# Optimization experiments

Measured on AMD Instinct MI355X. Metric: run time of the kernel, lower is better.

## Reference

```python
import jax, jax.numpy as jnp
import numpy as np

N_NODES = 50000
N_EDGES = 800000
D_IN, D_HID, D_OUT = 64, 128, 64


def _sage_conv(x, src, dst, W_l, b_l, W_r):
    # PyG SAGEConv (aggr='mean'): out = lin_l(mean_j x_j) + lin_r(x_i)
    msg = x[src]                                    # [E, d] gather
    summed = jax.ops.segment_sum(msg, dst, num_segments=N_NODES)
    cnt = jax.ops.segment_sum(jnp.ones((msg.shape[0], 1), x.dtype), dst,
                              num_segments=N_NODES)
    mean = summed / jnp.maximum(cnt, 1.0)           # [N, d]
    return mean @ W_l + b_l + x @ W_r


def setup_inputs() -> dict:
    key = jax.random.key(0)
    ks = jax.random.split(key, 8)
    x = jax.random.normal(ks[0], (N_NODES, D_IN), dtype=jnp.float32)
    edge_index = jax.random.randint(ks[1], (2, N_EDGES), 0, N_NODES, dtype=jnp.int64)
    s1 = 1.0 / np.sqrt(D_IN)
    s2 = 1.0 / np.sqrt(D_HID)
    W_l1 = jax.random.uniform(ks[2], (D_IN, D_HID), jnp.float32, -s1, s1)
    b_l1 = jnp.zeros((D_HID,), jnp.float32)
    W_r1 = jax.random.uniform(ks[3], (D_IN, D_HID), jnp.float32, -s1, s1)
    W_l2 = jax.random.uniform(ks[4], (D_HID, D_OUT), jnp.float32, -s2, s2)
    b_l2 = jnp.zeros((D_OUT,), jnp.float32)
    W_r2 = jax.random.uniform(ks[5], (D_HID, D_OUT), jnp.float32, -s2, s2)
    return {"x": x, "edge_index": edge_index,
            "W_l1": W_l1, "b_l1": b_l1, "W_r1": W_r1,
            "W_l2": W_l2, "b_l2": b_l2, "W_r2": W_r2}


def reference(x, edge_index, W_l1, b_l1, W_r1, W_l2, b_l2, W_r2):
    src, dst = edge_index[0], edge_index[1]
    h = _sage_conv(x, src, dst, W_l1, b_l1, W_r1)
    h = jax.nn.relu(h)
    # dropout is identity in eval mode (F.dropout(training=self.training))
    out = _sage_conv(h, src, dst, W_l2, b_l2, W_r2)
    return out
```

## Files before the change

kernel.cpp:

```cpp
#include <hip/hip_runtime.h>

namespace {

constexpr int NNODES = 50000;
constexpr int NEDGES = 800000;
constexpr int NBUCK  = (NNODES + 127) / 128;
constexpr int BCAP   = 3072;
constexpr int SB     = 64;
constexpr int CHUNK  = NEDGES / SB;
constexpr int CONVB  = 1024;


static __device__ __forceinline__ unsigned short f2bf(float f) {
  unsigned u = __float_as_uint(f);
  u += 0x7FFFu + ((u >> 16) & 1u);
  return (unsigned short)(u >> 16);
}
static __device__ __forceinline__ float bf2f(unsigned short b) {
  return __uint_as_float((unsigned)b << 16);
}

static __device__ __forceinline__ void pk_fma_lo(float2& d, const float2 a, const float2 b) {
  asm("v_pk_fma_f32 %0, %1, %2, %0 op_sel:[0,0,0] op_sel_hi:[0,1,1]"
      : "+v"(d) : "v"(a), "v"(b));
}
static __device__ __forceinline__ void pk_fma_hi(float2& d, const float2 a, const float2 b) {
  asm("v_pk_fma_f32 %0, %1, %2, %0 op_sel:[1,0,0] op_sel_hi:[1,1,1]"
      : "+v"(d) : "v"(a), "v"(b));
}

static __device__ __forceinline__ int detect_is64_block(const void* raw, int* s_tmp) {
  if (threadIdx.x == 0) *s_tmp = 0;
  __syncthreads();
  const unsigned int* w = (const unsigned int*)raw;
  const int nz = (w[1 + 2 * (int)(threadIdx.x & 511)] != 0u) ? 1 : 0;
  if (nz) atomicOr(s_tmp, 1);
  __syncthreads();
  return (*s_tmp == 0) ? 1 : 0;
}

__global__ __launch_bounds__(512) void histconv(const void* __restrict__ raw,
                                                const float* __restrict__ xin,
                                                unsigned short* __restrict__ xb,
                                                int* __restrict__ blkhist) {
  const int tid = (int)threadIdx.x;
  if (blockIdx.x >= SB) {
    const int b = blockIdx.x - SB;
    for (int t = b * 512 + tid; t < NNODES * 64 / 4; t += CONVB * 512) {
      const float4 v = ((const float4*)xin)[t];
      ushort4 o;
      o.x = f2bf(v.x); o.y = f2bf(v.y); o.z = f2bf(v.z); o.w = f2bf(v.w);
      ((ushort4*)xb)[t] = o;
    }
    return;
  }
  __shared__ int hist[NBUCK];
  __shared__ int s_tmp;
  const int is64 = detect_is64_block(raw, &s_tmp);
  for (int i = tid; i < NBUCK; i += 512) hist[i] = 0;
  __syncthreads();
  const int b = blockIdx.x;
  const int beg = b * CHUNK, end = beg + CHUNK;
  for (int e = beg + tid; e < end; e += 512) {
    const int d = is64 ? (int)((const long long*)raw)[NEDGES + e]
                       : ((const int*)raw)[NEDGES + e];
    atomicAdd(&hist[d >> 7], 1);
  }
  __syncthreads();
  for (int i = tid; i < NBUCK; i += 512) blkhist[i * SB + b] = hist[i];
}

__global__ __launch_bounds__(512) void scatter_pass(const void* __restrict__ raw,
                                                    const int* __restrict__ blkhist,
                                                    unsigned int* __restrict__ ecol) {
  __shared__ int loff[NBUCK];
  __shared__ int lcur[NBUCK];
  __shared__ int s_tmp;
  const int is64 = detect_is64_block(raw, &s_tmp);
  const int b = blockIdx.x;
  const int tid = (int)threadIdx.x;
  for (int bk = tid; bk < NBUCK; bk += 512) {
    int s = 0;
    for (int bb = 0; bb < b; ++bb) s += blkhist[bk * SB + bb];
    loff[bk] = bk * BCAP + s;
    lcur[bk] = 0;
  }
  __syncthreads();
  const int beg = b * CHUNK, end = beg + CHUNK;
  for (int e = beg + tid; e < end; e += 512) {
    int s, d;
    if (is64) {
      const long long* p = (const long long*)raw;
      s = (int)p[e];
      d = (int)p[NEDGES + e];
    } else {
      const int* p = (const int*)raw;
      s = p[e];
      d = p[NEDGES + e];
    }
    const int bk = d >> 7;
    const unsigned int val = ((unsigned int)d << 16) | (unsigned int)s;
    const int lr = atomicAdd(&lcur[bk], 1);
    ecol[loff[bk] + lr] = val;
  }
}

__global__ __launch_bounds__(256) void csr_emit(const int* __restrict__ blkhist,
                                                unsigned int* __restrict__ ecol,
                                                int* __restrict__ rowse) {
  const int bk = blockIdx.x;
  const int base = bk * 128;
  const int nloc = min(128, NNODES - base);
  const int tid = (int)threadIdx.x;
  unsigned int* eb = ecol + (size_t)bk * BCAP;

  __shared__ int dcnt[128];
  __shared__ int noff[128];
  __shared__ int ncur[128];
  __shared__ int s_cnt;
  if (tid < 64) {
    int c = blkhist[bk * SB + tid];
#pragma unroll
    for (int off = 32; off; off >>= 1) c += __shfl_down(c, off, 64);
    if (tid == 0) s_cnt = c;
  }
  if (tid < 128) dcnt[tid] = 0;
  __syncthreads();
  const int cnt = s_cnt;

  unsigned int vals[12];
  int m = 0;
#pragma unroll
  for (int k = 0; k < 12; ++k) {
    const int e = tid + k * 256;
    if (e < cnt) {
      vals[k] = eb[e];
      atomicAdd(&dcnt[(vals[k] >> 16) & 127u], 1);
      m = k + 1;
    }
  }
  __syncthreads();

  if (tid < 128) noff[tid] = dcnt[tid];
  __syncthreads();
#pragma unroll
  for (int off = 1; off < 128; off <<= 1) {
    int add = 0;
    if (tid < 128 && tid >= off) add = noff[tid - off];
    __syncthreads();
    if (tid < 128) noff[tid] += add;
    __syncthreads();
  }
  if (tid < 128) {
    const int excl = noff[tid] - dcnt[tid];
    noff[tid] = excl;
    ncur[tid] = 0;
    if (tid < nloc)
      rowse[base + tid] = ((bk * BCAP + excl) << 9) | dcnt[tid];
  }
  __syncthreads();

#pragma unroll
  for (int k = 0; k < 12; ++k) {
    if (k < m) {
      const int loc = (int)((vals[k] >> 16) & 127u);
      eb[noff[loc] + atomicAdd(&ncur[loc], 1)] = vals[k] & 0xFFFFu;
    }
  }
}

template <bool FINAL>
__global__ __launch_bounds__(256) void seg_mean_bf(const unsigned int* __restrict__ xb2,
                                                   const int* __restrict__ rowse,
                                                   const unsigned int* __restrict__ col,
                                                   const unsigned int* __restrict__ radd2,
                                                   float* __restrict__ outbuf) {
  const int lane = (int)(threadIdx.x & 63);
  const int half = lane >> 5;
  const int c = lane & 31;
  const int wid = (blockIdx.x * blockDim.x + threadIdx.x) >> 6;
  const int nw = (gridDim.x * blockDim.x) >> 6;
  for (int v = wid; v < NNODES; v += nw) {
    const int se = rowse[v];
    const int b = se >> 9;
    const int e = b + (se & 511);
    float accx = 0.0f, accy = 0.0f;
    int i = b;
    for (; i + 8 <= e; i += 8) {
      const int s0 = (int)col[i + 0 + half];
      const int s1 = (int)col[i + 2 + half];
      const int s2 = (int)col[i + 4 + half];
      const int s3 = (int)col[i + 6 + half];
      const unsigned int w0 = xb2[(size_t)s0 * 32 + c];
      const unsigned int w1 = xb2[(size_t)s1 * 32 + c];
      const unsigned int w2 = xb2[(size_t)s2 * 32 + c];
      const unsigned int w3 = xb2[(size_t)s3 * 32 + c];
      accx += __uint_as_float(w0 << 16) + __uint_as_float(w1 << 16)
            + __uint_as_float(w2 << 16) + __uint_as_float(w3 << 16);
      accy += __uint_as_float(w0 & 0xFFFF0000u) + __uint_as_float(w1 & 0xFFFF0000u)
            + __uint_as_float(w2 & 0xFFFF0000u) + __uint_as_float(w3 & 0xFFFF0000u);
    }
    for (; i + 2 <= e; i += 2) {
      const unsigned int w0 = xb2[(size_t)col[i + half] * 32 + c];
      accx += __uint_as_float(w0 << 16);
      accy += __uint_as_float(w0 & 0xFFFF0000u);
    }
    if (i < e && half == 0) {
      const unsigned int w0 = xb2[(size_t)col[i] * 32 + c];
      accx += __uint_as_float(w0 << 16);
      accy += __uint_as_float(w0 & 0xFFFF0000u);
    }
    accx += __shfl_xor(accx, 32, 64);
    accy += __shfl_xor(accy, 32, 64);
    if (half == 0) {
      const float inv = 1.0f / fmaxf((float)(se & 511), 1.0f);
      float2 res = make_float2(accx * inv, accy * inv);
      const size_t gi = (size_t)v * 32 + c;
      if (FINAL) {
        const unsigned int ra = radd2[gi];
        res.x += __uint_as_float(ra << 16);
        res.y += __uint_as_float(ra & 0xFFFF0000u);
      }
      ((float2*)outbuf)[gi] = res;
    }
  }
}

template <int MODE>
__global__ __launch_bounds__(256, 4) void gemm128(const float* __restrict__ A0,
                                                  const float* __restrict__ A1,
                                                  const unsigned short* __restrict__ AH,
                                                  const float* __restrict__ W0,
                                                  const float* __restrict__ W1,
                                                  const float* __restrict__ bias,
                                                  unsigned short* __restrict__ HB,
                                                  unsigned short* __restrict__ PB,
                                                  unsigned short* __restrict__ RB) {
  constexpr int SAS = 36;
  __shared__ float sA[64][SAS];
  __shared__ float sW[32][128];
  const int row0 = blockIdx.x * 64;
  const int tid = threadIdx.x;
  const int r0 = (tid >> 4) * 4;
  const int j0 = (tid & 15) * 4;

  float2 accA2[4][2];
  float2 accB2[4][2];
#pragma unroll
  for (int r = 0; r < 4; ++r)
#pragma unroll
    for (int p = 0; p < 2; ++p) {
      accA2[r][p] = make_float2(0.f, 0.f);
      accB2[r][p] = make_float2(0.f, 0.f);
    }

#pragma unroll 1
  for (int ck = 0; ck < 4; ++ck) {
#pragma unroll
    for (int v = 0; v < 2; ++v) {
      const int vid = v * 256 + tid;
      const int rr = vid >> 3;
      const int kq = (vid & 7) * 4;
      const int grow = row0 + rr;
      float4 val = make_float4(0.f, 0.f, 0.f, 0.f);
      if (grow < NNODES) {
        if (MODE == 0) {
          const float* src = (ck < 2) ? A0 : A1;
          const int kk = (ck & 1) * 32 + kq;
          val = *(const float4*)&src[(size_t)grow * 64 + kk];
        } else {
          const ushort4 us = *(const ushort4*)&AH[(size_t)grow * 128 + ck * 32 + kq];
          val = make_float4(bf2f(us.x), bf2f(us.y), bf2f(us.z), bf2f(us.w));
        }
      }
      *(float4*)&sA[rr][kq] = val;
    }
#pragma unroll
    for (int v = 0; v < 4; ++v) {
      const int vid = v * 256 + tid;
      const int kk = vid >> 5;
      const int jq = (vid & 31) * 4;
      float4 w;
      if (MODE == 0) {
        const float* src = (ck < 2) ? W0 : W1;
        const int krel = (ck & 1) * 32 + kk;
        w = *(const float4*)&src[(size_t)krel * 128 + jq];
      } else {
        const int kg = ck * 32 + kk;
        const float* src = (jq < 64) ? W0 : W1;
        const int jrel = (jq < 64) ? jq : jq - 64;
        w = *(const float4*)&src[(size_t)kg * 64 + jrel];
      }
      *(float4*)&sW[kk][jq] = w;
    }
    __syncthreads();
#pragma unroll
    for (int k4 = 0; k4 < 8; ++k4) {
      float4 a[4];
#pragma unroll
      for (int r = 0; r < 4; ++r) a[r] = *(const float4*)&sA[r0 + r][k4 * 4];
#pragma unroll
      for (int kp = 0; kp < 2; ++kp) {
        const int k_even = k4 * 4 + kp * 2;
        const float4 wlo0 = *(const float4*)&sW[k_even][j0];
        const float4 whi0 = *(const float4*)&sW[k_even][64 + j0];
        const float4 wlo1 = *(const float4*)&sW[k_even + 1][j0];
        const float4 whi1 = *(const float4*)&sW[k_even + 1][64 + j0];
#pragma unroll
        for (int r = 0; r < 4; ++r) {
          const float2 ap = (kp == 0) ? make_float2(a[r].x, a[r].y)
                                      : make_float2(a[r].z, a[r].w);
          pk_fma_lo(accA2[r][0], ap, make_float2(wlo0.x, wlo0.y));
          pk_fma_lo(accA2[r][1], ap, make_float2(wlo0.z, wlo0.w));
          pk_fma_lo(accB2[r][0], ap, make_float2(whi0.x, whi0.y));
          pk_fma_lo(accB2[r][1], ap, make_float2(whi0.z, whi0.w));
          pk_fma_hi(accA2[r][0], ap, make_float2(wlo1.x, wlo1.y));
          pk_fma_hi(accA2[r][1], ap, make_float2(wlo1.z, wlo1.w));
          pk_fma_hi(accB2[r][0], ap, make_float2(whi1.x, whi1.y));
          pk_fma_hi(accB2[r][1], ap, make_float2(whi1.z, whi1.w));
        }
      }
    }
    __syncthreads();
  }

  float4 blo = make_float4(0.f, 0.f, 0.f, 0.f);
  float4 bhi;
  if (MODE == 0) {
    blo = *(const float4*)&bias[j0];
    bhi = *(const float4*)&bias[64 + j0];
  } else {
    bhi = *(const float4*)&bias[j0];
  }
#pragma unroll
  for (int r = 0; r < 4; ++r) {
    const int grow = row0 + r0 + r;
    if (grow >= NNODES) continue;
    float4 lo = make_float4(accA2[r][0].x + blo.x, accA2[r][0].y + blo.y,
                            accA2[r][1].x + blo.z, accA2[r][1].y + blo.w);
    float4 hi = make_float4(accB2[r][0].x + bhi.x, accB2[r][0].y + bhi.y,
                            accB2[r][1].x + bhi.z, accB2[r][1].y + bhi.w);
    if (MODE == 0) {
      ushort4 olo, ohi;
      olo.x = f2bf(fmaxf(lo.x, 0.f)); olo.y = f2bf(fmaxf(lo.y, 0.f));
      olo.z = f2bf(fmaxf(lo.z, 0.f)); olo.w = f2bf(fmaxf(lo.w, 0.f));
      ohi.x = f2bf(fmaxf(hi.x, 0.f)); ohi.y = f2bf(fmaxf(hi.y, 0.f));
      ohi.z = f2bf(fmaxf(hi.z, 0.f)); ohi.w = f2bf(fmaxf(hi.w, 0.f));
      *(ushort4*)&HB[(size_t)grow * 128 + j0] = olo;
      *(ushort4*)&HB[(size_t)grow * 128 + 64 + j0] = ohi;
    } else {
      ushort4 op, orr;
      op.x = f2bf(lo.x); op.y = f2bf(lo.y); op.z = f2bf(lo.z); op.w = f2bf(lo.w);
      orr.x = f2bf(hi.x); orr.y = f2bf(hi.y); orr.z = f2bf(hi.z); orr.w = f2bf(hi.w);
      *(ushort4*)&PB[(size_t)grow * 64 + j0] = op;
      *(ushort4*)&RB[(size_t)grow * 64 + j0] = orr;
    }
  }
}

}

extern "C" void kernel_launch(void* const* d_in, const int* in_sizes, int n_in,
                              void* d_out, int out_size, void* d_ws, size_t ws_size,
                              hipStream_t stream) {
  const float* x   = (const float*)d_in[0];
  const void*  ei  = d_in[1];
  const float* Wl1 = (const float*)d_in[2];
  const float* bl1 = (const float*)d_in[3];
  const float* Wr1 = (const float*)d_in[4];
  const float* Wl2 = (const float*)d_in[5];
  const float* bl2 = (const float*)d_in[6];
  const float* Wr2 = (const float*)d_in[7];
  float* out = (float*)d_out;

  char* ws = (char*)d_ws;
  int*            blkhist = (int*)(ws + 0);
  int*            rowse   = (int*)(ws + 100352);
  unsigned int*   ecol    = (unsigned int*)(ws + 301056);
  unsigned short* xb      = (unsigned short*)(ws + 5105664);
  unsigned short* pb      = (unsigned short*)(ws + 11505664);
  float*          mean1   = (float*)(ws + 17905664);
  unsigned short* hb      = (unsigned short*)(ws + 30705664);
  unsigned short* rb      = (unsigned short*)(ws + 43505664);

  histconv<<<SB + CONVB, 512, 0, stream>>>(ei, x, xb, blkhist);
  scatter_pass<<<SB, 512, 0, stream>>>(ei, blkhist, ecol);
  csr_emit<<<NBUCK, 256, 0, stream>>>(blkhist, ecol, rowse);

  constexpr int GEMM_BLOCKS = (NNODES + 63) / 64;

  seg_mean_bf<false><<<12500, 256, 0, stream>>>((const unsigned int*)xb, rowse, ecol,
                                                nullptr, mean1);
  gemm128<0><<<GEMM_BLOCKS, 256, 0, stream>>>(mean1, x, nullptr, Wl1, Wr1, bl1,
                                              hb, nullptr, nullptr);
  gemm128<1><<<GEMM_BLOCKS, 256, 0, stream>>>(nullptr, nullptr, hb, Wl2, Wr2, bl2,
                                              nullptr, pb, rb);
  seg_mean_bf<true><<<12500, 256, 0, stream>>>((const unsigned int*)pb, rowse, ecol,
                                               (const unsigned int*)rb, out);
}
```

Baseline: 158.2 us.

## Replace FP32 FMA GEMMs with bf16 MFMA using split hi/lo weights

Both dense GEMMs now run on MFMA 16x16x32 bf16 instructions instead of scalar packed FP32 FMAs. Weights are pre-transposed and split into bf16 hi and lo parts inside the first kernel, so precision stays near FP32 for the weights. The first-layer mean aggregate is now written as bf16 rather than fp32, and layer 1 reads the bf16 copy of x, which halves those activation reads and writes. The cost is extra rounding on the activations and two MFMAs per k-step, and the weight B fragments are read straight from global memory.

```diff
diff --git a/kernel.cpp b/kernel.cpp
--- a/kernel.cpp
+++ b/kernel.cpp
@@ -11,6 +11,9 @@
 constexpr int CONVB  = 1024;
 
 
+typedef __attribute__((ext_vector_type(8))) short bf16x8;
+typedef __attribute__((ext_vector_type(4))) float f32x4;
+
 static __device__ __forceinline__ unsigned short f2bf(float f) {
   unsigned u = __float_as_uint(f);
   u += 0x7FFFu + ((u >> 16) & 1u);
@@ -20,15 +23,6 @@
   return __uint_as_float((unsigned)b << 16);
 }
 
-static __device__ __forceinline__ void pk_fma_lo(float2& d, const float2 a, const float2 b) {
-  asm("v_pk_fma_f32 %0, %1, %2, %0 op_sel:[0,0,0] op_sel_hi:[0,1,1]"
-      : "+v"(d) : "v"(a), "v"(b));
-}
-static __device__ __forceinline__ void pk_fma_hi(float2& d, const float2 a, const float2 b) {
-  asm("v_pk_fma_f32 %0, %1, %2, %0 op_sel:[1,0,0] op_sel_hi:[1,1,1]"
-      : "+v"(d) : "v"(a), "v"(b));
-}
-
 static __device__ __forceinline__ int detect_is64_block(const void* raw, int* s_tmp) {
   if (threadIdx.x == 0) *s_tmp = 0;
   __syncthreads();
@@ -41,9 +35,38 @@
 
 __global__ __launch_bounds__(512) void histconv(const void* __restrict__ raw,
                                                 const float* __restrict__ xin,
+                                                const float* __restrict__ Wl1,
+                                                const float* __restrict__ Wr1,
+                                                const float* __restrict__ Wl2,
+                                                const float* __restrict__ Wr2,
                                                 unsigned short* __restrict__ xb,
+                                                unsigned short* __restrict__ WT1hi,
+                                                unsigned short* __restrict__ WT1lo,
+                                                unsigned short* __restrict__ WT2hi,
+                                                unsigned short* __restrict__ WT2lo,
                                                 int* __restrict__ blkhist) {
   const int tid = (int)threadIdx.x;
+  if (blockIdx.x >= SB + CONVB) {
+    const int q = (int)blockIdx.x - (SB + CONVB);
+    const int layer = q >> 1;
+    const int jbase = (q & 1) * 64;
+    unsigned short* WH = layer ? WT2hi : WT1hi;
+    unsigned short* WL = layer ? WT2lo : WT1lo;
+    for (int t = tid; t < 64 * 128; t += 512) {
+      const int j = jbase + (t >> 7);
+      const int k = t & 127;
+      float wv;
+      if (layer == 0) wv = (k < 64) ? Wl1[(size_t)k * 128 + j]
+                                    : Wr1[(size_t)(k - 64) * 128 + j];
+      else            wv = (j < 64) ? Wl2[(size_t)k * 64 + j]
+                                    : Wr2[(size_t)k * 64 + (j - 64)];
+      const unsigned short hi = f2bf(wv);
+      const unsigned short lo = f2bf(wv - bf2f(hi));
+      WH[(size_t)j * 128 + k] = hi;
+      WL[(size_t)j * 128 + k] = lo;
+    }
+    return;
+  }
   if (blockIdx.x >= SB) {
     const int b = blockIdx.x - SB;
     for (int t = b * 512 + tid; t < NNODES * 64 / 4; t += CONVB * 512) {
@@ -174,7 +197,8 @@
                                                    const int* __restrict__ rowse,
                                                    const unsigned int* __restrict__ col,
                                                    const unsigned int* __restrict__ radd2,
-                                                   float* __restrict__ outbuf) {
+                                                   float* __restrict__ outf,
+                                                   unsigned int* __restrict__ outb) {
   const int lane = (int)(threadIdx.x & 63);
   const int half = lane >> 5;
   const int c = lane & 31;
@@ -220,140 +244,102 @@
         const unsigned int ra = radd2[gi];
         res.x += __uint_as_float(ra << 16);
         res.y += __uint_as_float(ra & 0xFFFF0000u);
+        ((float2*)outf)[gi] = res;
+      } else {
+        outb[gi] = ((unsigned)f2bf(res.y) << 16) | (unsigned)f2bf(res.x);
       }
-      ((float2*)outbuf)[gi] = res;
     }
   }
 }
 
 template <int MODE>
-__global__ __launch_bounds__(256, 4) void gemm128(const float* __restrict__ A0,
-                                                  const float* __restrict__ A1,
-                                                  const unsigned short* __restrict__ AH,
-                                                  const float* __restrict__ W0,
-                                                  const float* __restrict__ W1,
-                                                  const float* __restrict__ bias,
-                                                  unsigned short* __restrict__ HB,
-                                                  unsigned short* __restrict__ PB,
-                                                  unsigned short* __restrict__ RB) {
-  constexpr int SAS = 36;
-  __shared__ float sA[64][SAS];
-  __shared__ float sW[32][128];
+__global__ __launch_bounds__(256, 4) void gemm_mfma(const unsigned short* __restrict__ A0,
+                                                    const unsigned short* __restrict__ A1,
+                                                    const unsigned short* __restrict__ WThi,
+                                                    const unsigned short* __restrict__ WTlo,
+                                                    const float* __restrict__ bias,
+                                                    unsigned short* __restrict__ O0,
+                                                    unsigned short* __restrict__ O1) {
+  constexpr int LDA = 136;
+  constexpr int LDO = 132;
+  __shared__ unsigned short At[64 * LDA];
   const int row0 = blockIdx.x * 64;
-  const int tid = threadIdx.x;
-  const int r0 = (tid >> 4) * 4;
-  const int j0 = (tid & 15) * 4;
-
-  float2 accA2[4][2];
-  float2 accB2[4][2];
-#pragma unroll
-  for (int r = 0; r < 4; ++r)
-#pragma unroll
-    for (int p = 0; p < 2; ++p) {
-      accA2[r][p] = make_float2(0.f, 0.f);
-      accB2[r][p] = make_float2(0.f, 0.f);
-    }
+  const int tid = (int)threadIdx.x;
+
+#pragma unroll
+  for (int cc = 0; cc < 4; ++cc) {
+    const int chunk = cc * 256 + tid;
+    const int rr = chunk >> 4;
+    const int seg = chunk & 15;
+    const int grow = row0 + rr;
+    ushort4 v0 = make_ushort4(0, 0, 0, 0), v1 = make_ushort4(0, 0, 0, 0);
+    if (grow < NNODES) {
+      const unsigned short* src;
+      if (MODE == 0)
+        src = (seg < 8) ? &A0[(size_t)grow * 64 + seg * 8]
+                        : &A1[(size_t)grow * 64 + (seg - 8) * 8];
+      else
+        src = &A0[(size_t)grow * 128 + seg * 8];
+      v0 = *(const ushort4*)src;
+      v1 = *(const ushort4*)(src + 4);
+    }
+    *(ushort4*)&At[rr * LDA + seg * 8] = v0;
+    *(ushort4*)&At[rr * LDA + seg * 8 + 4] = v1;
+  }
+  __syncthreads();
+
+  const int w = tid >> 6;
+  const int l = tid & 63;
+  const int i16 = l & 15;
+  const int g = l >> 4;
+
+  bf16x8 af[4];
+#pragma unroll
+  for (int ks = 0; ks < 4; ++ks)
+    af[ks] = *(const bf16x8*)&At[(w * 16 + i16) * LDA + ks * 32 + g * 8];
+  __syncthreads();
 
 #pragma unroll 1
-  for (int ck = 0; ck < 4; ++ck) {
-#pragma unroll
-    for (int v = 0; v < 2; ++v) {
-      const int vid = v * 256 + tid;
-      const int rr = vid >> 3;
-      const int kq = (vid & 7) * 4;
-      const int grow = row0 + rr;
-      float4 val = make_float4(0.f, 0.f, 0.f, 0.f);
-      if (grow < NNODES) {
-        if (MODE == 0) {
-          const float* src = (ck < 2) ? A0 : A1;
-          const int kk = (ck & 1) * 32 + kq;
-          val = *(const float4*)&src[(size_t)grow * 64 + kk];
-        } else {
-          const ushort4 us = *(const ushort4*)&AH[(size_t)grow * 128 + ck * 32 + kq];
-          val = make_float4(bf2f(us.x), bf2f(us.y), bf2f(us.z), bf2f(us.w));
-        }
-      }
-      *(float4*)&sA[rr][kq] = val;
-    }
-#pragma unroll
-    for (int v = 0; v < 4; ++v) {
-      const int vid = v * 256 + tid;
-      const int kk = vid >> 5;
-      const int jq = (vid & 31) * 4;
-      float4 w;
-      if (MODE == 0) {
-        const float* src = (ck < 2) ? W0 : W1;
-        const int krel = (ck & 1) * 32 + kk;
-        w = *(const float4*)&src[(size_t)krel * 128 + jq];
-      } else {
-        const int kg = ck * 32 + kk;
-        const float* src = (jq < 64) ? W0 : W1;
-        const int jrel = (jq < 64) ? jq : jq - 64;
-        w = *(const float4*)&src[(size_t)kg * 64 + jrel];
-      }
-      *(float4*)&sW[kk][jq] = w;
-    }
-    __syncthreads();
-#pragma unroll
-    for (int k4 = 0; k4 < 8; ++k4) {
-      float4 a[4];
-#pragma unroll
-      for (int r = 0; r < 4; ++r) a[r] = *(const float4*)&sA[r0 + r][k4 * 4];
-#pragma unroll
-      for (int kp = 0; kp < 2; ++kp) {
-        const int k_even = k4 * 4 + kp * 2;
-        const float4 wlo0 = *(const float4*)&sW[k_even][j0];
-        const float4 whi0 = *(const float4*)&sW[k_even][64 + j0];
-        const float4 wlo1 = *(const float4*)&sW[k_even + 1][j0];
-        const float4 whi1 = *(const float4*)&sW[k_even + 1][64 + j0];
-#pragma unroll
-        for (int r = 0; r < 4; ++r) {
-          const float2 ap = (kp == 0) ? make_float2(a[r].x, a[r].y)
-                                      : make_float2(a[r].z, a[r].w);
-          pk_fma_lo(accA2[r][0], ap, make_float2(wlo0.x, wlo0.y));
-          pk_fma_lo(accA2[r][1], ap, make_float2(wlo0.z, wlo0.w));
-          pk_fma_lo(accB2[r][0], ap, make_float2(whi0.x, whi0.y));
-          pk_fma_lo(accB2[r][1], ap, make_float2(whi0.z, whi0.w));
-          pk_fma_hi(accA2[r][0], ap, make_float2(wlo1.x, wlo1.y));
-          pk_fma_hi(accA2[r][1], ap, make_float2(wlo1.z, wlo1.w));
-          pk_fma_hi(accB2[r][0], ap, make_float2(whi1.x, whi1.y));
-          pk_fma_hi(accB2[r][1], ap, make_float2(whi1.z, whi1.w));
-        }
-      }
-    }
-    __syncthreads();
-  }
-
-  float4 blo = make_float4(0.f, 0.f, 0.f, 0.f);
-  float4 bhi;
-  if (MODE == 0) {
-    blo = *(const float4*)&bias[j0];
-    bhi = *(const float4*)&bias[64 + j0];
-  } else {
-    bhi = *(const float4*)&bias[j0];
-  }
-#pragma unroll
-  for (int r = 0; r < 4; ++r) {
-    const int grow = row0 + r0 + r;
+  for (int ct = 0; ct < 8; ++ct) {
+    f32x4 acc = {0.f, 0.f, 0.f, 0.f};
+    const size_t wb = (size_t)(ct * 16 + i16) * 128 + g * 8;
+#pragma unroll
+    for (int ks = 0; ks < 4; ++ks) {
+      const bf16x8 bh = *(const bf16x8*)&WThi[wb + ks * 32];
+      acc = __builtin_amdgcn_mfma_f32_16x16x32_bf16(af[ks], bh, acc, 0, 0, 0);
+      const bf16x8 bl = *(const bf16x8*)&WTlo[wb + ks * 32];
+      acc = __builtin_amdgcn_mfma_f32_16x16x32_bf16(af[ks], bl, acc, 0, 0, 0);
+    }
+    const int colc = ct * 16 + i16;
+    float bsc = 0.f;
+    if (MODE == 0) bsc = bias[colc];
+    else if (colc >= 64) bsc = bias[colc - 64];
+#pragma unroll
+    for (int e = 0; e < 4; ++e) {
+      float v = acc[e] + bsc;
+      if (MODE == 0) v = fmaxf(v, 0.f);
+      At[(w * 16 + g * 4 + e) * LDO + colc] = f2bf(v);
+    }
+  }
+  __syncthreads();
+
+#pragma unroll
+  for (int cc = 0; cc < 4; ++cc) {
+    const int chunk = cc * 256 + tid;
+    const int rr = chunk >> 4;
+    const int seg = chunk & 15;
+    const int grow = row0 + rr;
     if (grow >= NNODES) continue;
-    float4 lo = make_float4(accA2[r][0].x + blo.x, accA2[r][0].y + blo.y,
-                            accA2[r][1].x + blo.z, accA2[r][1].y + blo.w);
-    float4 hi = make_float4(accB2[r][0].x + bhi.x, accB2[r][0].y + bhi.y,
-                            accB2[r][1].x + bhi.z, accB2[r][1].y + bhi.w);
+    ushort4 v0 = *(const ushort4*)&At[rr * LDO + seg * 8];
+    ushort4 v1 = *(const ushort4*)&At[rr * LDO + seg * 8 + 4];
     if (MODE == 0) {
-      ushort4 olo, ohi;
-      olo.x = f2bf(fmaxf(lo.x, 0.f)); olo.y = f2bf(fmaxf(lo.y, 0.f));
-      olo.z = f2bf(fmaxf(lo.z, 0.f)); olo.w = f2bf(fmaxf(lo.w, 0.f));
-      ohi.x = f2bf(fmaxf(hi.x, 0.f)); ohi.y = f2bf(fmaxf(hi.y, 0.f));
-      ohi.z = f2bf(fmaxf(hi.z, 0.f)); ohi.w = f2bf(fmaxf(hi.w, 0.f));
-      *(ushort4*)&HB[(size_t)grow * 128 + j0] = olo;
-      *(ushort4*)&HB[(size_t)grow * 128 + 64 + j0] = ohi;
+      *(ushort4*)&O0[(size_t)grow * 128 + seg * 8] = v0;
+      *(ushort4*)&O0[(size_t)grow * 128 + seg * 8 + 4] = v1;
     } else {
-      ushort4 op, orr;
-      op.x = f2bf(lo.x); op.y = f2bf(lo.y); op.z = f2bf(lo.z); op.w = f2bf(lo.w);
-      orr.x = f2bf(hi.x); orr.y = f2bf(hi.y); orr.z = f2bf(hi.z); orr.w = f2bf(hi.w);
-      *(ushort4*)&PB[(size_t)grow * 64 + j0] = op;
-      *(ushort4*)&RB[(size_t)grow * 64 + j0] = orr;
+      unsigned short* dst = (seg < 8) ? &O0[(size_t)grow * 64 + seg * 8]
+                                      : &O1[(size_t)grow * 64 + (seg - 8) * 8];
+      *(ushort4*)dst = v0;
+      *(ushort4*)(dst + 4) = v1;
     }
   }
 }
@@ -379,22 +365,28 @@
   unsigned int*   ecol    = (unsigned int*)(ws + 301056);
   unsigned short* xb      = (unsigned short*)(ws + 5105664);
   unsigned short* pb      = (unsigned short*)(ws + 11505664);
-  float*          mean1   = (float*)(ws + 17905664);
-  unsigned short* hb      = (unsigned short*)(ws + 30705664);
-  unsigned short* rb      = (unsigned short*)(ws + 43505664);
-
-  histconv<<<SB + CONVB, 512, 0, stream>>>(ei, x, xb, blkhist);
+  unsigned short* mb      = (unsigned short*)(ws + 17905664);
+  unsigned short* hb      = (unsigned short*)(ws + 24305664);
+  unsigned short* rb      = (unsigned short*)(ws + 37105664);
+  unsigned short* WT1hi   = (unsigned short*)(ws + 43505664);
+  unsigned short* WT1lo   = (unsigned short*)(ws + 43538432);
+  unsigned short* WT2hi   = (unsigned short*)(ws + 43571200);
+  unsigned short* WT2lo   = (unsigned short*)(ws + 43603968);
+
+  histconv<<<SB + CONVB + 4, 512, 0, stream>>>(ei, x, Wl1, Wr1, Wl2, Wr2,
+                                               xb, WT1hi, WT1lo, WT2hi, WT2lo,
+                                               blkhist);
   scatter_pass<<<SB, 512, 0, stream>>>(ei, blkhist, ecol);
   csr_emit<<<NBUCK, 256, 0, stream>>>(blkhist, ecol, rowse);
 
   constexpr int GEMM_BLOCKS = (NNODES + 63) / 64;
 
   seg_mean_bf<false><<<12500, 256, 0, stream>>>((const unsigned int*)xb, rowse, ecol,
-                                                nullptr, mean1);
-  gemm128<0><<<GEMM_BLOCKS, 256, 0, stream>>>(mean1, x, nullptr, Wl1, Wr1, bl1,
-                                              hb, nullptr, nullptr);
-  gemm128<1><<<GEMM_BLOCKS, 256, 0, stream>>>(nullptr, nullptr, hb, Wl2, Wr2, bl2,
-                                              nullptr, pb, rb);
+                                                nullptr, nullptr, (unsigned int*)mb);
+  gemm_mfma<0><<<GEMM_BLOCKS, 256, 0, stream>>>(mb, xb, WT1hi, WT1lo, bl1,
+                                                hb, nullptr);
+  gemm_mfma<1><<<GEMM_BLOCKS, 256, 0, stream>>>(hb, nullptr, WT2hi, WT2lo, bl2,
+                                                pb, rb);
   seg_mean_bf<true><<<12500, 256, 0, stream>>>((const unsigned int*)pb, rowse, ecol,
-                                               (const unsigned int*)rb, out);
-}
+                                               (const unsigned int*)rb, out, nullptr);
+}
```

After: 163.1 us. +3.1%, slower.
